# Optimization experiments

Measured on AMD Instinct MI355X. Metric: run time of the kernel, lower is better.

Reference implementation:

```python
import jax, jax.numpy as jnp
import numpy as np

B_J0 = 0.01
LENS = 0.5
GAMMA = 0.5
BETA = 1.8
R_M = 1.0
DT = 1.0


@jax.custom_vjp
def act_fun_adp(x):
    return (x > 0).astype(x.dtype)

def _act_fwd(x):
    return (x > 0).astype(x.dtype), x

def _act_bwd(x, g):
    # Gaussian surrogate gradient (config.gradient_type == 'G')
    temp = jnp.exp(-x ** 2 / (2 * LENS ** 2)) / jnp.sqrt(2 * jnp.pi) / LENS
    return (g * temp * GAMMA,)

act_fun_adp.defvjp(_act_fwd, _act_bwd)


def setup_inputs() -> dict:
    key = jax.random.key(0)
    ks = jax.random.split(key, 20)
    B, T, I, H, O = 256, 250, 700, 512, 20
    inp = {}
    inp['input'] = (jax.random.uniform(ks[0], (B, T, I)) < 0.1).astype(jnp.float32)  # sparse spikes
    inp['mask'] = (jax.random.uniform(ks[1], (2, H, H)) < 0.8).astype(jnp.float32)
    inp['hid1_mem0'] = jax.random.uniform(ks[2], (B, H)) * 0.1
    inp['hid2_mem0'] = jax.random.uniform(ks[3], (B, H)) * 0.1
    inp['out_mem0'] = jax.random.uniform(ks[4], (B, O)) * 0.1
    # parameters (xavier-ish init)
    def xav(k, shape):
        lim = np.sqrt(6.0 / (shape[0] + shape[1]))
        return jax.random.uniform(k, shape, minval=-lim, maxval=lim)
    inp['W_in'] = xav(ks[5], (H, I)); inp['b_in'] = jnp.zeros((H,))
    inp['W_h11'] = 0.2 * xav(ks[6], (H, H)); inp['b_h11'] = jnp.zeros((H,))
    inp['W_h12'] = xav(ks[7], (H, H)); inp['b_h12'] = jnp.zeros((H,))
    inp['W_h22'] = 0.2 * xav(ks[8], (H, H)); inp['b_h22'] = jnp.zeros((H,))
    inp['W_out'] = xav(ks[9], (O, H)); inp['b_o'] = jnp.zeros((O,))
    inp['tau_adp_h1'] = 150.0 + 10.0 * jax.random.normal(ks[10], (H,))
    inp['tau_adp_h2'] = 150.0 + 10.0 * jax.random.normal(ks[11], (H,))
    inp['tau_m_h1'] = 20.0 + 5.0 * jax.random.normal(ks[12], (H,))
    inp['tau_m_h2'] = 20.0 + 5.0 * jax.random.normal(ks[13], (H,))
    inp['tau_m_o'] = 20.0 + 5.0 * jax.random.normal(ks[14], (O,))
    return inp


def reference(input, mask, hid1_mem0, hid2_mem0, out_mem0,
              W_in, b_in, W_h11, b_h11, W_h12, b_h12, W_h22, b_h22,
              W_out, b_o, tau_adp_h1, tau_adp_h2, tau_m_h1, tau_m_h2, tau_m_o):
    T = input.shape[1]
    # recurrent weights masked once before the time loop (weight.data *= mask.T)
    W_h11e = W_h11 * mask[0].T
    W_h22e = W_h22 * mask[1].T
    # per-neuron decay factors (constant across time)
    alpha1 = jnp.exp(-DT / tau_m_h1)
    alpha2 = jnp.exp(-DT / tau_m_h2)
    alpha_o = jnp.exp(-DT / tau_m_o)
    ro1 = jnp.exp(-DT / tau_adp_h1)
    ro2 = jnp.exp(-DT / tau_adp_h2)

    xs = jnp.transpose(input, (1, 0, 2))  # [T, B, I]

    def step(carry, x_t):
        mem1, spk1, mem2, spk2, outm, acc, s1, s2 = carry
        # layer 1 (note: b fed in is always b_j0, matching the torch code)
        b1 = ro1 * B_J0 + (1 - ro1) * spk1
        B1 = B_J0 + BETA * b1
        i1 = x_t @ W_in.T + b_in + spk1 @ W_h11e.T + b_h11
        mem1 = mem1 * alpha1 + (1 - alpha1) * R_M * i1 - B1 * spk1 * DT
        spk1 = act_fun_adp(mem1 - B1)
        # layer 2
        b2 = ro2 * B_J0 + (1 - ro2) * spk2
        B2 = B_J0 + BETA * b2
        i2 = spk1 @ W_h12.T + b_h12 + spk2 @ W_h22e.T + b_h22
        mem2 = mem2 * alpha2 + (1 - alpha2) * R_M * i2 - B2 * spk2 * DT
        spk2 = act_fun_adp(mem2 - B2)
        # leaky-integrator readout (no spike)
        io = spk2 @ W_out.T + b_o
        outm = outm * alpha_o + (1 - alpha_o) * R_M * io
        acc = acc + jax.nn.softmax(outm, axis=1)
        return (mem1, spk1, mem2, spk2, outm, acc, s1 + spk1, s2 + spk2), None

    B = input.shape[0]
    H = W_in.shape[0]
    O = W_out.shape[0]
    carry0 = (hid1_mem0, jnp.zeros((B, H)), hid2_mem0, jnp.zeros((B, H)),
              out_mem0, jnp.zeros((B, O)), jnp.zeros((B, H)), jnp.zeros((B, H)))
    carry, _ = jax.lax.scan(step, carry0, xs)
    _, _, _, _, _, output, s1, s2 = carry
    A_norm = jnp.sum(jnp.abs(W_h11e)) + jnp.sum(jnp.abs(W_h22e))
    return output, s1 / T, s2 / T, A_norm
```

## Files before the change

### kernel.cpp

```cpp
#include <hip/hip_runtime.h>

constexpr int BATCH = 256;
constexpr int TSTEPS = 250;
constexpr int NI = 700;
constexpr int NH = 512;
constexpr int NO = 20;

constexpr int OFF_WIN = 0;
constexpr int OFF_W11 = NI * NH;
constexpr int OFF_W12 = OFF_W11 + NH * NH;
constexpr int OFF_W22 = OFF_W12 + NH * NH;

#define B_J0  0.01f
#define BETA_ 1.8f

__global__ void transpose_mask(const float* __restrict__ in, const float* __restrict__ mask,
                               float* __restrict__ out, int R, int C) {
    __shared__ float tile[32][33];
    int cb = blockIdx.x * 32, rb = blockIdx.y * 32;
    int tx = threadIdx.x, ty = threadIdx.y;
    #pragma unroll
    for (int i = 0; i < 32; i += 8) {
        int r = rb + ty + i, c = cb + tx;
        if (r < R && c < C) tile[ty + i][tx] = in[(size_t)r * C + c];
    }
    __syncthreads();
    #pragma unroll
    for (int i = 0; i < 32; i += 8) {
        int c = cb + ty + i, r = rb + tx;
        if (c < C && r < R) {
            float v = tile[tx][ty + i];
            if (mask) v *= mask[(size_t)c * R + r];
            out[(size_t)c * R + r] = v;
        }
    }
}

__global__ void transpose_wout(const float* __restrict__ in, float* __restrict__ out) {
    int idx = blockIdx.x * blockDim.x + threadIdx.x;
    if (idx < NH * NO) {
        int j = idx / NO, o = idx % NO;
        out[idx] = in[o * NH + j];
    }
}

__global__ void anorm_stage1(const float* __restrict__ Wh11, const float* __restrict__ Wh22,
                             const float* __restrict__ mask, float* __restrict__ partial) {
    __shared__ float red[256];
    int tid = threadIdx.x;
    float s = 0.f;
    for (int idx = blockIdx.x * 256 + tid; idx < NH * NH; idx += 256 * 128) {
        int hh = idx / NH, j = idx % NH;
        s += fabsf(Wh11[idx] * mask[j * NH + hh]);
        s += fabsf(Wh22[idx] * mask[NH * NH + j * NH + hh]);
    }
    red[tid] = s;
    __syncthreads();
    for (int st = 128; st > 0; st >>= 1) {
        if (tid < st) red[tid] += red[tid + st];
        __syncthreads();
    }
    if (tid == 0) partial[blockIdx.x] = red[0];
}

__global__ void anorm_stage2(const float* __restrict__ partial, float* __restrict__ out) {
    __shared__ float red[128];
    int tid = threadIdx.x;
    red[tid] = partial[tid];
    __syncthreads();
    for (int st = 64; st > 0; st >>= 1) {
        if (tid < st) red[tid] += red[tid + st];
        __syncthreads();
    }
    if (tid == 0) out[0] = red[0];
}

__device__ __forceinline__ void f4add(float4& a, const float4 b) {
    a.x += b.x; a.y += b.y; a.z += b.z; a.w += b.w;
}

__device__ __forceinline__ float4 gather8(const int* __restrict__ list, int kb, int ke,
                                          const float* __restrict__ W, int q) {
    float4 a0{0,0,0,0}, a1{0,0,0,0}, a2{0,0,0,0}, a3{0,0,0,0},
           a4{0,0,0,0}, a5{0,0,0,0}, a6{0,0,0,0}, a7{0,0,0,0};
    int k = kb;
    const int q4 = q << 2;
    for (; k + 7 < ke; k += 8) {
        int o0 = list[k],     o1 = list[k + 1], o2 = list[k + 2], o3 = list[k + 3];
        int o4 = list[k + 4], o5 = list[k + 5], o6 = list[k + 6], o7 = list[k + 7];
        float4 v0 = *reinterpret_cast<const float4*>(W + o0 + q4);
        float4 v1 = *reinterpret_cast<const float4*>(W + o1 + q4);
        float4 v2 = *reinterpret_cast<const float4*>(W + o2 + q4);
        float4 v3 = *reinterpret_cast<const float4*>(W + o3 + q4);
        float4 v4 = *reinterpret_cast<const float4*>(W + o4 + q4);
        float4 v5 = *reinterpret_cast<const float4*>(W + o5 + q4);
        float4 v6 = *reinterpret_cast<const float4*>(W + o6 + q4);
        float4 v7 = *reinterpret_cast<const float4*>(W + o7 + q4);
        f4add(a0, v0); f4add(a1, v1); f4add(a2, v2); f4add(a3, v3);
        f4add(a4, v4); f4add(a5, v5); f4add(a6, v6); f4add(a7, v7);
    }
    for (; k < ke; ++k)
        f4add(a0, *reinterpret_cast<const float4*>(W + list[k] + q4));
    f4add(a0, a1); f4add(a2, a3); f4add(a4, a5); f4add(a6, a7);
    f4add(a0, a2); f4add(a4, a6); f4add(a0, a4);
    return a0;
}

__global__ __launch_bounds__(NH, 2) void snn_kernel(
    const float* __restrict__ input,
    const float* __restrict__ h1m0, const float* __restrict__ h2m0, const float* __restrict__ om0,
    const float* __restrict__ b_in, const float* __restrict__ b_h11,
    const float* __restrict__ b_h12, const float* __restrict__ b_h22,
    const float* __restrict__ b_o,
    const float* __restrict__ tau_adp_h1, const float* __restrict__ tau_adp_h2,
    const float* __restrict__ tau_m_h1, const float* __restrict__ tau_m_h2,
    const float* __restrict__ tau_m_o,
    const float* __restrict__ ws, const float* __restrict__ WoutT,
    float* __restrict__ out)
{
    __shared__ int actA[NH + NI];
    __shared__ int actB[2 * NH];
    __shared__ int cnt1[8], cnt2[8], cntA[8], cntB[8];
    __shared__ float4 part4a[4 * 128];
    __shared__ float4 part4b[4 * 128];
    __shared__ float part[320];

    const int tid = threadIdx.x;
    const int b = blockIdx.x;
    const int h = tid;
    const int s = tid >> 7;
    const int q = tid & 127;
    const int lane = tid & 63;
    const int w = tid >> 6;
    const unsigned long long ltmask = (1ull << lane) - 1ull;
    const bool hasTail = tid < (NI - NH);

    float mem1 = h1m0[b * NH + h];
    float mem2 = h2m0[b * NH + h];
    float spk1 = 0.f, spk2 = 0.f, s1c = 0.f, s2c = 0.f;
    const float al1 = expf(-1.f / tau_m_h1[h]);
    const float al2 = expf(-1.f / tau_m_h2[h]);
    const float ro1 = expf(-1.f / tau_adp_h1[h]);
    const float ro2 = expf(-1.f / tau_adp_h2[h]);
    const float bs1 = b_in[h] + b_h11[h];
    const float bs2 = b_h12[h] + b_h22[h];

    float outm = 0.f, accO = 0.f, alo = 0.f, bo = 0.f;
    if (tid < NO) {
        outm = om0[b * NO + tid];
        alo = expf(-1.f / tau_m_o[tid]);
        bo = b_o[tid];
    }

    const float* xbase = input + (size_t)b * TSTEPS * NI;

    int lenA = 0, lenB = 0;
    {
        float xc0 = __builtin_nontemporal_load(xbase + tid);
        float xc1 = hasTail ? __builtin_nontemporal_load(xbase + NH + tid) : 0.f;
        unsigned long long mA = __ballot(xc0 > 0.f);
        unsigned long long mB = __ballot(hasTail && xc1 > 0.f);
        if (lane == 0) { cntA[w] = __popcll(mA); cntB[w] = __popcll(mB); }
        __syncthreads();
        int oA = 0, nA = 0, oB = 0, nB = 0;
        #pragma unroll
        for (int i = 0; i < 8; ++i) {
            int ca = cntA[i], cb = cntB[i];
            if (i < w) { oA += ca; oB += cb; }
            nA += ca; nB += cb;
        }
        if (xc0 > 0.f) actA[oA + __popcll(mA & ltmask)] = OFF_WIN + (tid << 9);
        if (hasTail && xc1 > 0.f) actA[nA + oB + __popcll(mB & ltmask)] = OFF_WIN + ((NH + tid) << 9);
        lenA = nA + nB;
        __syncthreads();
    }

    for (int k = 0; k <= TSTEPS; ++k) {
        const bool hasNext = (k + 1) < TSTEPS;
        float xn0 = 0.f, xn1 = 0.f;
        if (hasNext) {
            const float* xn = xbase + (size_t)(k + 1) * NI;
            xn0 = __builtin_nontemporal_load(xn + tid);
            xn1 = hasTail ? __builtin_nontemporal_load(xn + NH + tid) : 0.f;
        }

        if (k < TSTEPS) {
            float4 pa = gather8(actA, (lenA * s) >> 2, (lenA * (s + 1)) >> 2, ws, q);
            part4a[(s << 7) + q] = pa;
        }
        if (k > 0) {
            float4 pb = gather8(actB, (lenB * s) >> 2, (lenB * (s + 1)) >> 2, ws, q);
            part4b[(s << 7) + q] = pb;
        }
        __syncthreads();

        const float* pfa = (const float*)part4a;
        const float* pfb = (const float*)part4b;
        float ns1 = 0.f, ns2 = 0.f;
        if (k < TSTEPS) {
            float i1 = ((pfa[h] + pfa[NH + h]) + (pfa[2 * NH + h] + pfa[3 * NH + h])) + bs1;
            float b1 = ro1 * B_J0 + (1.f - ro1) * spk1;
            float B1 = B_J0 + BETA_ * b1;
            mem1 = mem1 * al1 + (1.f - al1) * i1 - B1 * spk1;
            ns1 = (mem1 - B1) > 0.f ? 1.f : 0.f;
            spk1 = ns1; s1c += ns1;
        }
        if (k > 0) {
            float i2 = ((pfb[h] + pfb[NH + h]) + (pfb[2 * NH + h] + pfb[3 * NH + h])) + bs2;
            float b2 = ro2 * B_J0 + (1.f - ro2) * spk2;
            float B2 = B_J0 + BETA_ * b2;
            mem2 = mem2 * al2 + (1.f - al2) * i2 - B2 * spk2;
            ns2 = (mem2 - B2) > 0.f ? 1.f : 0.f;
            spk2 = ns2; s2c += ns2;
        }
        unsigned long long m1 = __ballot(ns1 != 0.f);
        unsigned long long m2 = __ballot(ns2 != 0.f);
        bool fA = hasNext && (xn0 > 0.f);
        bool fB = hasNext && hasTail && (xn1 > 0.f);
        unsigned long long mA = __ballot(fA);
        unsigned long long mB = __ballot(fB);
        if (lane == 0) {
            cnt1[w] = __popcll(m1); cnt2[w] = __popcll(m2);
            cntA[w] = __popcll(mA); cntB[w] = __popcll(mB);
        }
        __syncthreads();

        int o1 = 0, n1 = 0, o2 = 0, n2 = 0, oA = 0, nA = 0, oB = 0, nB = 0;
        #pragma unroll
        for (int i = 0; i < 8; ++i) {
            int c1 = cnt1[i], c2 = cnt2[i], ca = cntA[i], cb = cntB[i];
            if (i < w) { o1 += c1; o2 += c2; oA += ca; oB += cb; }
            n1 += c1; n2 += c2; nA += ca; nB += cb;
        }
        if (ns1 != 0.f) {
            int p1 = o1 + __popcll(m1 & ltmask);
            actA[p1] = OFF_W11 + (h << 9);
            actB[p1] = OFF_W12 + (h << 9);
        }
        if (ns2 != 0.f)
            actB[n1 + o2 + __popcll(m2 & ltmask)] = OFF_W22 + (h << 9);
        if (fA) actA[n1 + oA + __popcll(mA & ltmask)] = OFF_WIN + (tid << 9);
        if (fB) actA[n1 + nA + oB + __popcll(mB & ltmask)] = OFF_WIN + ((NH + tid) << 9);
        lenA = n1 + nA + nB;
        lenB = n1 + n2;
        __syncthreads();

        if (k > 0) {
            if (tid < 320) {
                int o = tid % NO, r = tid / NO;
                float p = 0.f;
                for (int kk = r; kk < n2; kk += 16) {
                    int j = (actB[n1 + kk] - OFF_W22) >> 9;
                    p += WoutT[j * NO + o];
                }
                part[tid] = p;
            }
            __syncthreads();
            if (tid < 64) {
                float io = bo, v = -__builtin_huge_valf(), e = 0.f;
                if (tid < NO) {
                    #pragma unroll
                    for (int r = 0; r < 16; ++r) io += part[r * NO + tid];
                    outm = outm * alo + (1.f - alo) * io;
                    v = outm;
                }
                float mx = v;
                #pragma unroll
                for (int off = 16; off > 0; off >>= 1) mx = fmaxf(mx, __shfl_xor(mx, off, 32));
                if (tid < NO) e = expf(outm - mx);
                float ssum = e;
                #pragma unroll
                for (int off = 16; off > 0; off >>= 1) ssum += __shfl_xor(ssum, off, 32);
                if (tid < NO) accO += e / ssum;
            }
        }
    }

    if (tid < NO) out[b * NO + tid] = accO;
    out[BATCH * NO + (size_t)b * NH + h] = s1c * (1.f / TSTEPS);
    out[BATCH * NO + BATCH * NH + (size_t)b * NH + h] = s2c * (1.f / TSTEPS);
}

extern "C" void kernel_launch(void* const* d_in, const int* in_sizes, int n_in,
                              void* d_out, int out_size, void* d_ws, size_t ws_size,
                              hipStream_t stream) {
    const float* input      = (const float*)d_in[0];
    const float* mask       = (const float*)d_in[1];
    const float* h1m0       = (const float*)d_in[2];
    const float* h2m0       = (const float*)d_in[3];
    const float* om0        = (const float*)d_in[4];
    const float* W_in       = (const float*)d_in[5];
    const float* b_in       = (const float*)d_in[6];
    const float* W_h11      = (const float*)d_in[7];
    const float* b_h11      = (const float*)d_in[8];
    const float* W_h12      = (const float*)d_in[9];
    const float* b_h12      = (const float*)d_in[10];
    const float* W_h22      = (const float*)d_in[11];
    const float* b_h22      = (const float*)d_in[12];
    const float* W_out      = (const float*)d_in[13];
    const float* b_o        = (const float*)d_in[14];
    const float* tau_adp_h1 = (const float*)d_in[15];
    const float* tau_adp_h2 = (const float*)d_in[16];
    const float* tau_m_h1   = (const float*)d_in[17];
    const float* tau_m_h2   = (const float*)d_in[18];
    const float* tau_m_o    = (const float*)d_in[19];

    float* out = (float*)d_out;
    float* ws  = (float*)d_ws;

    float* WinT  = ws + OFF_WIN;
    float* Wh11T = ws + OFF_W11;
    float* Wh12T = ws + OFF_W12;
    float* Wh22T = ws + OFF_W22;
    float* WoutT = Wh22T + NH * NH;
    float* apart = WoutT + NH * NO;

    dim3 tb(32, 8);
    transpose_mask<<<dim3((NI + 31) / 32, (NH + 31) / 32), tb, 0, stream>>>(W_in, nullptr, WinT, NH, NI);
    transpose_mask<<<dim3(16, 16), tb, 0, stream>>>(W_h11, mask,            Wh11T, NH, NH);
    transpose_mask<<<dim3(16, 16), tb, 0, stream>>>(W_h12, nullptr,         Wh12T, NH, NH);
    transpose_mask<<<dim3(16, 16), tb, 0, stream>>>(W_h22, mask + NH * NH,  Wh22T, NH, NH);
    transpose_wout<<<(NH * NO + 255) / 256, 256, 0, stream>>>(W_out, WoutT);
    anorm_stage1<<<128, 256, 0, stream>>>(W_h11, W_h22, mask, apart);
    anorm_stage2<<<1, 128, 0, stream>>>(apart, out + BATCH * NO + 2 * BATCH * NH);

    snn_kernel<<<BATCH, NH, 0, stream>>>(input, h1m0, h2m0, om0,
        b_in, b_h11, b_h12, b_h22, b_o,
        tau_adp_h1, tau_adp_h2, tau_m_h1, tau_m_h2, tau_m_o,
        ws, WoutT, out);
}
```

Measured before the change: 1.464 ms.

## Widen SNN block to 768 threads and defer readout one step

The per-batch block grows from 512 to 768 threads, so the sparse weight gather is split across six slices instead of four, and each input column gets its own thread instead of a two-pass tail. The readout/softmax for step k is deferred to iteration k+1, where it overlaps with the gathers. This removes one or two block barriers per time step. In exchange each block needs more registers and shared memory, the loop runs one extra iteration, and occupancy per CU may drop under the new launch bounds.

```diff
diff --git a/kernel.cpp b/kernel.cpp
--- a/kernel.cpp
+++ b/kernel.cpp
@@ -5,6 +5,9 @@
 constexpr int NI = 700;
 constexpr int NH = 512;
 constexpr int NO = 20;
+constexpr int NT = 768;
+constexpr int NWAVE = 12;
+constexpr int NSLICE = 6;
 
 constexpr int OFF_WIN = 0;
 constexpr int OFF_W11 = NI * NH;
@@ -106,7 +109,7 @@
     return a0;
 }
 
-__global__ __launch_bounds__(NH, 2) void snn_kernel(
+__global__ __launch_bounds__(NT, 3) void snn_kernel(
     const float* __restrict__ input,
     const float* __restrict__ h1m0, const float* __restrict__ h2m0, const float* __restrict__ om0,
     const float* __restrict__ b_in, const float* __restrict__ b_h11,
@@ -120,9 +123,9 @@
 {
     __shared__ int actA[NH + NI];
     __shared__ int actB[2 * NH];
-    __shared__ int cnt1[8], cnt2[8], cntA[8], cntB[8];
-    __shared__ float4 part4a[4 * 128];
-    __shared__ float4 part4b[4 * 128];
+    __shared__ int cnt1[NWAVE], cnt2[NWAVE], cntI[NWAVE];
+    __shared__ float4 part4a[NSLICE * 128];
+    __shared__ float4 part4b[NSLICE * 128];
     __shared__ float part[320];
 
     const int tid = threadIdx.x;
@@ -133,17 +136,21 @@
     const int lane = tid & 63;
     const int w = tid >> 6;
     const unsigned long long ltmask = (1ull << lane) - 1ull;
-    const bool hasTail = tid < (NI - NH);
-
-    float mem1 = h1m0[b * NH + h];
-    float mem2 = h2m0[b * NH + h];
-    float spk1 = 0.f, spk2 = 0.f, s1c = 0.f, s2c = 0.f;
-    const float al1 = expf(-1.f / tau_m_h1[h]);
-    const float al2 = expf(-1.f / tau_m_h2[h]);
-    const float ro1 = expf(-1.f / tau_adp_h1[h]);
-    const float ro2 = expf(-1.f / tau_adp_h2[h]);
-    const float bs1 = b_in[h] + b_h11[h];
-    const float bs2 = b_h12[h] + b_h22[h];
+    const bool isN = tid < NH;
+    const bool isI = tid < NI;
+
+    float mem1 = 0.f, mem2 = 0.f, spk1 = 0.f, spk2 = 0.f, s1c = 0.f, s2c = 0.f;
+    float al1 = 0.f, al2 = 0.f, ro1 = 0.f, ro2 = 0.f, bs1 = 0.f, bs2 = 0.f;
+    if (isN) {
+        mem1 = h1m0[b * NH + h];
+        mem2 = h2m0[b * NH + h];
+        al1 = expf(-1.f / tau_m_h1[h]);
+        al2 = expf(-1.f / tau_m_h2[h]);
+        ro1 = expf(-1.f / tau_adp_h1[h]);
+        ro2 = expf(-1.f / tau_adp_h2[h]);
+        bs1 = b_in[h] + b_h11[h];
+        bs2 = b_h12[h] + b_h22[h];
+    }
 
     float outm = 0.f, accO = 0.f, alo = 0.f, bo = 0.f;
     if (tid < NO) {
@@ -154,59 +161,64 @@
 
     const float* xbase = input + (size_t)b * TSTEPS * NI;
 
-    int lenA = 0, lenB = 0;
+    int lenA = 0, lenB = 0, prevN1 = 0, prevN2 = 0;
     {
-        float xc0 = __builtin_nontemporal_load(xbase + tid);
-        float xc1 = hasTail ? __builtin_nontemporal_load(xbase + NH + tid) : 0.f;
-        unsigned long long mA = __ballot(xc0 > 0.f);
-        unsigned long long mB = __ballot(hasTail && xc1 > 0.f);
-        if (lane == 0) { cntA[w] = __popcll(mA); cntB[w] = __popcll(mB); }
-        __syncthreads();
-        int oA = 0, nA = 0, oB = 0, nB = 0;
+        float xc = isI ? __builtin_nontemporal_load(xbase + tid) : 0.f;
+        unsigned long long mI = __ballot(xc > 0.f);
+        if (lane == 0) cntI[w] = __popcll(mI);
+        __syncthreads();
+        int oI = 0, nI = 0;
         #pragma unroll
-        for (int i = 0; i < 8; ++i) {
-            int ca = cntA[i], cb = cntB[i];
-            if (i < w) { oA += ca; oB += cb; }
-            nA += ca; nB += cb;
-        }
-        if (xc0 > 0.f) actA[oA + __popcll(mA & ltmask)] = OFF_WIN + (tid << 9);
-        if (hasTail && xc1 > 0.f) actA[nA + oB + __popcll(mB & ltmask)] = OFF_WIN + ((NH + tid) << 9);
-        lenA = nA + nB;
-        __syncthreads();
-    }
-
-    for (int k = 0; k <= TSTEPS; ++k) {
+        for (int i = 0; i < NWAVE; ++i) {
+            int ci = cntI[i];
+            if (i < w) oI += ci;
+            nI += ci;
+        }
+        if (xc > 0.f) actA[oI + __popcll(mI & ltmask)] = OFF_WIN + (tid << 9);
+        lenA = nI;
+        __syncthreads();
+    }
+
+    for (int k = 0; k <= TSTEPS + 1; ++k) {
         const bool hasNext = (k + 1) < TSTEPS;
-        float xn0 = 0.f, xn1 = 0.f;
-        if (hasNext) {
-            const float* xn = xbase + (size_t)(k + 1) * NI;
-            xn0 = __builtin_nontemporal_load(xn + tid);
-            xn1 = hasTail ? __builtin_nontemporal_load(xn + NH + tid) : 0.f;
-        }
+        float xn = 0.f;
+        if (hasNext && isI)
+            xn = __builtin_nontemporal_load(xbase + (size_t)(k + 1) * NI + tid);
 
         if (k < TSTEPS) {
-            float4 pa = gather8(actA, (lenA * s) >> 2, (lenA * (s + 1)) >> 2, ws, q);
+            float4 pa = gather8(actA, (lenA * s) / NSLICE, (lenA * (s + 1)) / NSLICE, ws, q);
             part4a[(s << 7) + q] = pa;
         }
-        if (k > 0) {
-            float4 pb = gather8(actB, (lenB * s) >> 2, (lenB * (s + 1)) >> 2, ws, q);
+        if (k >= 1 && k <= TSTEPS) {
+            float4 pb = gather8(actB, (lenB * s) / NSLICE, (lenB * (s + 1)) / NSLICE, ws, q);
             part4b[(s << 7) + q] = pb;
+        }
+        if (k >= 2 && tid < 320) {
+            int o = tid % NO, r = tid / NO;
+            float p = 0.f;
+            for (int kk = r; kk < prevN2; kk += 16) {
+                int j = (actB[prevN1 + kk] - OFF_W22) >> 9;
+                p += WoutT[j * NO + o];
+            }
+            part[tid] = p;
         }
         __syncthreads();
 
         const float* pfa = (const float*)part4a;
         const float* pfb = (const float*)part4b;
         float ns1 = 0.f, ns2 = 0.f;
-        if (k < TSTEPS) {
-            float i1 = ((pfa[h] + pfa[NH + h]) + (pfa[2 * NH + h] + pfa[3 * NH + h])) + bs1;
+        if (k < TSTEPS && isN) {
+            float i1 = (((pfa[h] + pfa[NH + h]) + (pfa[2 * NH + h] + pfa[3 * NH + h])) +
+                        (pfa[4 * NH + h] + pfa[5 * NH + h])) + bs1;
             float b1 = ro1 * B_J0 + (1.f - ro1) * spk1;
             float B1 = B_J0 + BETA_ * b1;
             mem1 = mem1 * al1 + (1.f - al1) * i1 - B1 * spk1;
             ns1 = (mem1 - B1) > 0.f ? 1.f : 0.f;
             spk1 = ns1; s1c += ns1;
         }
-        if (k > 0) {
-            float i2 = ((pfb[h] + pfb[NH + h]) + (pfb[2 * NH + h] + pfb[3 * NH + h])) + bs2;
+        if (k >= 1 && k <= TSTEPS && isN) {
+            float i2 = (((pfb[h] + pfb[NH + h]) + (pfb[2 * NH + h] + pfb[3 * NH + h])) +
+                        (pfb[4 * NH + h] + pfb[5 * NH + h])) + bs2;
             float b2 = ro2 * B_J0 + (1.f - ro2) * spk2;
             float B2 = B_J0 + BETA_ * b2;
             mem2 = mem2 * al2 + (1.f - al2) * i2 - B2 * spk2;
@@ -215,22 +227,36 @@
         }
         unsigned long long m1 = __ballot(ns1 != 0.f);
         unsigned long long m2 = __ballot(ns2 != 0.f);
-        bool fA = hasNext && (xn0 > 0.f);
-        bool fB = hasNext && hasTail && (xn1 > 0.f);
-        unsigned long long mA = __ballot(fA);
-        unsigned long long mB = __ballot(fB);
+        bool fI = hasNext && isI && (xn > 0.f);
+        unsigned long long mI = __ballot(fI);
         if (lane == 0) {
-            cnt1[w] = __popcll(m1); cnt2[w] = __popcll(m2);
-            cntA[w] = __popcll(mA); cntB[w] = __popcll(mB);
-        }
-        __syncthreads();
-
-        int o1 = 0, n1 = 0, o2 = 0, n2 = 0, oA = 0, nA = 0, oB = 0, nB = 0;
+            cnt1[w] = __popcll(m1); cnt2[w] = __popcll(m2); cntI[w] = __popcll(mI);
+        }
+        if (k >= 2 && tid < 64) {
+            float io = bo, v = -__builtin_huge_valf(), e = 0.f;
+            if (tid < NO) {
+                #pragma unroll
+                for (int r = 0; r < 16; ++r) io += part[r * NO + tid];
+                outm = outm * alo + (1.f - alo) * io;
+                v = outm;
+            }
+            float mx = v;
+            #pragma unroll
+            for (int off = 16; off > 0; off >>= 1) mx = fmaxf(mx, __shfl_xor(mx, off, 32));
+            if (tid < NO) e = expf(outm - mx);
+            float ssum = e;
+            #pragma unroll
+            for (int off = 16; off > 0; off >>= 1) ssum += __shfl_xor(ssum, off, 32);
+            if (tid < NO) accO += e / ssum;
+        }
+        __syncthreads();
+
+        int o1 = 0, n1 = 0, o2 = 0, n2 = 0, oI = 0, nI = 0;
         #pragma unroll
-        for (int i = 0; i < 8; ++i) {
-            int c1 = cnt1[i], c2 = cnt2[i], ca = cntA[i], cb = cntB[i];
-            if (i < w) { o1 += c1; o2 += c2; oA += ca; oB += cb; }
-            n1 += c1; n2 += c2; nA += ca; nB += cb;
+        for (int i = 0; i < NWAVE; ++i) {
+            int c1 = cnt1[i], c2 = cnt2[i], ci = cntI[i];
+            if (i < w) { o1 += c1; o2 += c2; oI += ci; }
+            n1 += c1; n2 += c2; nI += ci;
         }
         if (ns1 != 0.f) {
             int p1 = o1 + __popcll(m1 & ltmask);
@@ -239,46 +265,18 @@
         }
         if (ns2 != 0.f)
             actB[n1 + o2 + __popcll(m2 & ltmask)] = OFF_W22 + (h << 9);
-        if (fA) actA[n1 + oA + __popcll(mA & ltmask)] = OFF_WIN + (tid << 9);
-        if (fB) actA[n1 + nA + oB + __popcll(mB & ltmask)] = OFF_WIN + ((NH + tid) << 9);
-        lenA = n1 + nA + nB;
+        if (fI) actA[n1 + oI + __popcll(mI & ltmask)] = OFF_WIN + (tid << 9);
+        lenA = n1 + nI;
         lenB = n1 + n2;
-        __syncthreads();
-
-        if (k > 0) {
-            if (tid < 320) {
-                int o = tid % NO, r = tid / NO;
-                float p = 0.f;
-                for (int kk = r; kk < n2; kk += 16) {
-                    int j = (actB[n1 + kk] - OFF_W22) >> 9;
-                    p += WoutT[j * NO + o];
-                }
-                part[tid] = p;
-            }
-            __syncthreads();
-            if (tid < 64) {
-                float io = bo, v = -__builtin_huge_valf(), e = 0.f;
-                if (tid < NO) {
-                    #pragma unroll
-                    for (int r = 0; r < 16; ++r) io += part[r * NO + tid];
-                    outm = outm * alo + (1.f - alo) * io;
-                    v = outm;
-                }
-                float mx = v;
-                #pragma unroll
-                for (int off = 16; off > 0; off >>= 1) mx = fmaxf(mx, __shfl_xor(mx, off, 32));
-                if (tid < NO) e = expf(outm - mx);
-                float ssum = e;
-                #pragma unroll
-                for (int off = 16; off > 0; off >>= 1) ssum += __shfl_xor(ssum, off, 32);
-                if (tid < NO) accO += e / ssum;
-            }
-        }
+        prevN1 = n1; prevN2 = n2;
+        __syncthreads();
     }
 
     if (tid < NO) out[b * NO + tid] = accO;
-    out[BATCH * NO + (size_t)b * NH + h] = s1c * (1.f / TSTEPS);
-    out[BATCH * NO + BATCH * NH + (size_t)b * NH + h] = s2c * (1.f / TSTEPS);
+    if (isN) {
+        out[BATCH * NO + (size_t)b * NH + h] = s1c * (1.f / TSTEPS);
+        out[BATCH * NO + BATCH * NH + (size_t)b * NH + h] = s2c * (1.f / TSTEPS);
+    }
 }
 
 extern "C" void kernel_launch(void* const* d_in, const int* in_sizes, int n_in,
@@ -324,7 +322,7 @@
     anorm_stage1<<<128, 256, 0, stream>>>(W_h11, W_h22, mask, apart);
     anorm_stage2<<<1, 128, 0, stream>>>(apart, out + BATCH * NO + 2 * BATCH * NH);
 
-    snn_kernel<<<BATCH, NH, 0, stream>>>(input, h1m0, h2m0, om0,
+    snn_kernel<<<BATCH, NT, 0, stream>>>(input, h1m0, h2m0, om0,
         b_in, b_h11, b_h12, b_h22, b_o,
         tau_adp_h1, tau_adp_h2, tau_m_h1, tau_m_h2, tau_m_o,
         ws, WoutT, out);
```

Result: faster. 1.390 ms, median of 2 (-5.0%).
